# Kernel tuning notes

Measured on AMD Instinct MI355X. Metric: run time of the kernel, lower is better.

Reference implementation:

```python
import jax, jax.numpy as jnp
import numpy as np

N_HIDDEN = 512
BATCH = 16
MAX_LEN = 4096


def setup_inputs() -> dict:
    key = jax.random.key(0)
    k1, k2, k3 = jax.random.split(key, 3)
    h = jax.random.normal(k1, (BATCH, N_HIDDEN, MAX_LEN), dtype=jnp.float32)
    # Conv1d weight [out_ch=3*nh, in_ch=nh, kernel=2], fan-in scaled
    W = jax.random.normal(k2, (3 * N_HIDDEN, N_HIDDEN, 2), dtype=jnp.float32) / np.float32(np.sqrt(2.0 * N_HIDDEN))
    b = 0.02 * jax.random.normal(k3, (3 * N_HIDDEN,), dtype=jnp.float32)
    b = b.at[2 * N_HIDDEN:].set(1.0)  # init_gate_bias on the gate third of the bias
    # lengths: grouped (unique_consecutive) and sorted descending, padded into width MAX_LEN
    N = jnp.array([4096] * 4 + [3000] * 4 + [2048] * 4 + [1000] * 4, dtype=jnp.int32)
    return {"h": h, "W": W, "b": b, "N": N}


def _conv_reduce(h, W, b):
    # _reduce: Conv1d(nh -> 3*nh, kernel=2, stride=2) then gated combine (dropout=0).
    B, C, L = h.shape
    Lp = L + (L % 2)
    x = jnp.pad(h, ((0, 0), (0, 0), (0, Lp - L))).reshape(B, C, Lp // 2, 2)
    lrg = jnp.einsum('bclk,ock->bol', x, W) + b[None, :, None]  # [B, 3C, L//2]
    l = lrg[:, :C]
    r = jnp.tanh(lrg[:, C:2 * C])
    g = jax.nn.sigmoid(lrg[:, 2 * C:])
    return l * g + r * (1.0 - g)


def _forward(h, W, b, N):
    B, nh, L = h.shape
    # Nfp2 = largest power of two <= N ; M = 2*(N - Nfp2)
    Nfp2 = (2 ** jnp.floor(jnp.log2(N.astype(jnp.float32)))).astype(N.dtype)
    M = 2 * (N - Nfp2)
    # --- prefix reduce + suffix cat (padded/masked equivalent of _suffix_cat) ---
    # conv is local (k=2, s=2), so reducing the full padded width gives identical
    # values at the kept positions j < M//2.
    red = _conv_reduce(h, W, b)                      # [B, nh, ceil(L/2)]
    red = jnp.pad(red, ((0, 0), (0, 0), (0, L - red.shape[-1])))
    j = jnp.arange(L)
    half = (M // 2)[:, None]                         # [B, 1]
    take_red = j[None, :] < half                     # first M//2 slots <- reduced prefix
    idx = jnp.where(take_red, j[None, :], jnp.minimum(j[None, :] + half, L - 1))
    suf = jnp.take_along_axis(h, jnp.broadcast_to(idx[:, None, :], (B, nh, L)), axis=2)
    cur = jnp.where(take_red[:, None, :], red, suf)  # per-seq length now Nfp2 (power of 2)
    n = Nfp2
    # --- halving tree reduction; freeze sequences that reached length 1 ---
    steps = int(np.floor(np.log2(L)))
    for _ in range(steps):
        red = _conv_reduce(cur, W, b)
        neww = red.shape[-1]
        active = (n > 1)[:, None, None]
        cur = jnp.where(active, red, cur[:, :, :neww])
        n = jnp.where(n > 1, n // 2, n)
    return cur[:, :, 0]  # squeeze(-1) -> [B, nh]


def reference(h, W, b, N):
    return _forward(h, W, b, N)
```

## Files before the change

### kernel.cpp

```cpp
#include <hip/hip_runtime.h>

#define BATCH 16
#define CH 512
#define OC 1536
#define KDIM 1024
#define LMAX 4096
#define WGLOB_SZ 3145728

typedef __attribute__((ext_vector_type(8))) _Float16 h8v;
typedef __attribute__((ext_vector_type(4))) float f4v;

__device__ __forceinline__ int nfp2_of(int n) { return 1 << (31 - __clz(n)); }

__device__ __forceinline__ unsigned short h2u(_Float16 h) {
  union { _Float16 h; unsigned short u; } v; v.h = h; return v.u;
}

__device__ __forceinline__ void layout(const int* __restrict__ Nvec, int b,
                                       size_t& offC0, size_t& offA, size_t& offB,
                                       int& n, int& nfp2, int& half) {
  size_t c0t = 0, at = 0, bt = 0, c0o = 0, ao = 0, bo = 0;
  n = 2; nfp2 = 2; half = 0;
#pragma unroll 1
  for (int i = 0; i < BATCH; ++i) {
    int ni = Nvec[i];
    int f = nfp2_of(ni);
    int hf = ni - f;
    size_t cs = (size_t)((hf + 127) & ~127) << 11;
    size_t as = (size_t)(f >> 1) << 11;
    size_t bs = (size_t)(f >> 2) << 11;
    if (i < b) { c0o += cs; ao += as; bo += bs; }
    if (i == b) { n = ni; nfp2 = f; half = hf; }
    c0t += cs; at += as; bt += bs;
  }
  offC0 = (size_t)WGLOB_SZ + c0o;
  offA = (size_t)WGLOB_SZ + c0t + ao;
  offB = (size_t)WGLOB_SZ + c0t + at + bo;
}

__device__ __forceinline__ void gload16(const void* g, void* l) {
  __builtin_amdgcn_global_load_lds((const __attribute__((address_space(1))) void*)g,
                                   (__attribute__((address_space(3))) void*)l, 16, 0, 0);
}

__global__ __launch_bounds__(256) void prep_w_k(const float* __restrict__ W, char* __restrict__ ws) {
  int idx = blockIdx.x * 256 + threadIdx.x;
  if (idx >= 16 * 1536) return;
  int step = idx / 1536;
  int o = idx - step * 1536;
  const float* src = W + (size_t)o * KDIM + step * 64;
  unsigned short hb[64];
#pragma unroll
  for (int t = 0; t < 64; ++t) hb[t] = h2u((_Float16)src[t]);
  uint4* d4 = (uint4*)(ws + ((size_t)idx << 7));
#pragma unroll
  for (int s = 0; s < 8; ++s) {
    int oc = (s ^ (o & 7)) * 8;
    uint4 v;
    v.x = (unsigned)hb[oc + 0] | ((unsigned)hb[oc + 1] << 16);
    v.y = (unsigned)hb[oc + 2] | ((unsigned)hb[oc + 3] << 16);
    v.z = (unsigned)hb[oc + 4] | ((unsigned)hb[oc + 5] << 16);
    v.w = (unsigned)hb[oc + 6] | ((unsigned)hb[oc + 7] << 16);
    d4[s] = v;
  }
}

__global__ __launch_bounds__(256) void reorg_h_k(const float* __restrict__ h,
                                                 const int* __restrict__ Nvec,
                                                 char* __restrict__ ws,
                                                 float* __restrict__ dout, int mode) {
  __shared__ char T[32 * 256];
  const int b = blockIdx.z;
  size_t offC0, offA, offB; int n, nfp2, half;
  layout(Nvec, b, offC0, offA, offB, n, nfp2, half);
  const int tid = threadIdx.x;
  const int by = blockIdx.y;
  const int c0 = by * 64;

  if (mode == 1 && nfp2 == 1) {
    if (blockIdx.x == 0 && tid < 64)
      dout[(size_t)b * CH + c0 + tid] = h[(size_t)b * CH * LMAX + (size_t)(c0 + tid) * LMAX];
    return;
  }

  const int d0 = blockIdx.x * 32;
  int dlo, dhi, soff;
  size_t base;
  if (mode == 0) { dlo = 0; dhi = half; soff = 0; base = offC0; }
  else { dlo = half >> 1; dhi = nfp2 >> 1; soff = half; base = offA; }
  if (d0 >= dhi || d0 + 32 <= dlo) return;

  const float* hb = h + (size_t)b * CH * LMAX;

#pragma unroll
  for (int q = 0; q < 8; ++q) {
    int id = q * 256 + tid;
    int cl = id >> 5;
    int dl = id & 31;
    int d = d0 + dl;
    bool ok = (d < dhi) && (d >= dlo);
    float2 v;
    v.x = 0.f; v.y = 0.f;
    if (ok) v = *(const float2*)(hb + (size_t)(c0 + cl) * LMAX + 2 * d + soff);
    unsigned u = (unsigned)h2u((_Float16)v.x) | ((unsigned)h2u((_Float16)v.y) << 16);
    int g = cl >> 2;
    *(unsigned*)(T + dl * 256 + ((g ^ (dl & 15)) << 4) + (cl & 3) * 4) = u;
  }
  __syncthreads();
#pragma unroll
  for (int qq = 0; qq < 2; ++qq) {
    int gid = qq * 256 + tid;
    int dl = gid >> 4;
    int s = gid & 15;
    int d = d0 + dl;
    if (d >= dhi || d < dlo) continue;
    uint4 val = *(const uint4*)(T + dl * 256 + ((s ^ (dl & 15)) << 4));
    size_t dst = base + ((size_t)d << 11) + (size_t)((2 * by + (s >> 3)) << 7) +
                 (((s & 7) ^ (d & 7)) << 4);
    *(uint4*)(ws + dst) = val;
  }
}

__global__ __launch_bounds__(256, 2) void mfma_level_k(const float* __restrict__ bias,
                                                       const int* __restrict__ Nvec,
                                                       char* __restrict__ ws,
                                                       float* __restrict__ dout,
                                                       int level, int tiles) {
  __shared__ char smem[81920];
  const int id = blockIdx.x;
  const int o0 = (id & 7) * 64;
  const int r2 = id >> 3;
  const int xb = r2 % tiles;
  const int b = r2 / tiles;
  if (b >= BATCH) return;

  size_t offC0, offA, offB; int n, nfp2, half;
  layout(Nvec, b, offC0, offA, offB, n, nfp2, half);

  int cols;
  size_t inOff, outOff;
  if (level == 0) {
    if (half == 0) return;
    cols = half;
    inOff = offC0;
    outOff = offA;
  } else {
    int w = nfp2 >> (level - 1);
    if (w < 2) return;
    cols = w >> 1;
    inOff = (level & 1) ? offA : offB;
    outOff = (level & 1) ? offB : offA;
  }
  const bool fin = (level > 0) && ((nfp2 >> level) == 1);
  const int l0 = xb * 128;
  if (l0 >= cols) return;

  const int tid = threadIdx.x;
  const int lane = tid & 63, wid = tid >> 6;
  const int lane15 = lane & 15, lq = lane >> 4;
  const int rg = wid & 1, cg = wid >> 1;
  const char* inp = ws + inOff;

  unsigned aoff[6]; int adst[6];
#pragma unroll
  for (int q = 0; q < 6; ++q) {
    int d = q * 4096 + tid * 16;
    int r = d >> 7;
    int p = d & 127;
    int o = ((r >> 6) << 9) + o0 + (r & 63);
    aoff[q] = ((unsigned)o << 7) + p;
    adst[q] = q * 4096 + wid * 1024;
  }
  unsigned boff[4]; int bdst[4];
#pragma unroll
  for (int q = 0; q < 4; ++q) {
    int d = q * 4096 + tid * 16;
    int l = d >> 7;
    int p = d & 127;
    int lc = l0 + l; if (lc > cols - 1) lc = cols - 1;
    boff[q] = ((unsigned)lc << 11) + p;
    bdst[q] = q * 4096 + wid * 1024;
  }

#define STAGE(st, sel) do {                                                  \
    char* Ab = smem + (sel) * 24576;                                         \
    char* Bb = smem + 49152 + (sel) * 16384;                                 \
    unsigned ka = (unsigned)(st) * 196608u;                                  \
    unsigned kb = (unsigned)(st) << 7;                                       \
    _Pragma("unroll") for (int q = 0; q < 6; ++q)                            \
      gload16(ws + ka + aoff[q], Ab + adst[q]);                              \
    _Pragma("unroll") for (int q = 0; q < 4; ++q)                            \
      gload16(inp + kb + boff[q], Bb + bdst[q]);                             \
  } while (0)

  f4v acc[6][4];
#pragma unroll
  for (int m = 0; m < 6; ++m)
#pragma unroll
    for (int cf = 0; cf < 4; ++cf) acc[m][cf] = (f4v){0.f, 0.f, 0.f, 0.f};

  STAGE(0, 0);
  __syncthreads();

#pragma unroll 1
  for (int st = 0; st < 16; ++st) {
    const int cur = st & 1;
    if (st + 1 < 16) STAGE(st + 1, cur ^ 1);
    const char* Asb = smem + cur * 24576;
    const char* Bsb = smem + 49152 + cur * 16384;

#pragma unroll
    for (int s2 = 0; s2 < 2; ++s2) {
      const int oct = (s2 << 2) | lq;
      h8v bh[4];
#pragma unroll
      for (int cf = 0; cf < 4; ++cf) {
        int ll = cg * 64 + cf * 16 + lane15;
        bh[cf] = *(const h8v*)(Bsb + ll * 128 + ((oct ^ (ll & 7)) << 4));
      }
#pragma unroll
      for (int m = 0; m < 6; ++m) {
        int rr = (m >> 1) * 64 + rg * 32 + (m & 1) * 16 + lane15;
        h8v ah = *(const h8v*)(Asb + rr * 128 + ((oct ^ (rr & 7)) << 4));
#pragma unroll
        for (int cf = 0; cf < 4; ++cf)
          acc[m][cf] = __builtin_amdgcn_mfma_f32_16x16x32_f16(ah, bh[cf], acc[m][cf], 0, 0, 0);
      }
    }
    __syncthreads();
  }
#undef STAGE

  char* outp = ws + outOff;
#pragma unroll
  for (int s = 0; s < 2; ++s) {
#pragma unroll
    for (int cf = 0; cf < 4; ++cf) {
      f4v vl = acc[s][cf], vr = acc[2 + s][cf], vg = acc[4 + s][cf];
      int l = l0 + cg * 64 + cf * 16 + lane15;
      if (l >= cols) continue;
      int P = l >> 1, par = l & 1;
#pragma unroll
      for (int j = 0; j < 4; ++j) {
        int c = o0 + rg * 32 + s * 16 + lq * 4 + j;
        float zl = vl[j] + bias[c];
        float zr = vr[j] + bias[CH + c];
        float zg = vg[j] + bias[2 * CH + c];
        float g = 1.f / (1.f + __expf(-zg));
        float rt = 1.f - 2.f / (1.f + __expf(2.f * zr));
        float val = zl * g + rt * (1.f - g);
        if (fin) {
          if (l == 0) dout[(size_t)b * CH + c] = val;
        } else {
          int k = 2 * c + par;
          size_t byte = ((size_t)P << 11) + (size_t)((k >> 6) << 7) +
                        ((((k >> 3) & 7) ^ (P & 7)) << 4) + ((k & 7) << 1);
          *(unsigned short*)(outp + byte) = h2u((_Float16)val);
        }
      }
    }
  }
}

__global__ __launch_bounds__(256, 2) void small_level_k(const float* __restrict__ bias,
                                                        const int* __restrict__ Nvec,
                                                        char* __restrict__ ws,
                                                        float* __restrict__ dout,
                                                        int level, int tiles) {
  __shared__ char smem[131072];
  const int id = blockIdx.x;
  const int o0 = (id & 7) * 64;
  const int r2 = id >> 3;
  const int xb = r2 % tiles;
  const int b = r2 / tiles;
  if (b >= BATCH) return;

  size_t offC0, offA, offB; int n, nfp2, half;
  layout(Nvec, b, offC0, offA, offB, n, nfp2, half);

  int w = nfp2 >> (level - 1);
  if (w < 2) return;
  const int cols = w >> 1;
  const size_t inOff = (level & 1) ? offA : offB;
  const size_t outOff = (level & 1) ? offB : offA;
  const bool fin = (cols == 1);
  const int l0 = xb * 64;
  if (l0 >= cols) return;

  const int tid = threadIdx.x;
  const int lane = tid & 63, wid = tid >> 6;
  const int lane15 = lane & 15, lq = lane >> 4;
  const int rg = wid & 1, cg = wid >> 1;
  const char* inp = ws + inOff;

  unsigned aoff[12]; int adst[12];
#pragma unroll
  for (int q = 0; q < 12; ++q) {
    int d = q * 4096 + tid * 16;
    int r = d >> 8;
    int p = d & 255;
    int o = ((r >> 6) << 9) + o0 + (r & 63);
    aoff[q] = (unsigned)(p >> 7) * 196608u + ((unsigned)o << 7) + (p & 127);
    adst[q] = q * 4096 + wid * 1024;
  }
  unsigned boff[4]; int bdst[4];
#pragma unroll
  for (int q = 0; q < 4; ++q) {
    int d = q * 4096 + tid * 16;
    int l = d >> 8;
    int p = d & 255;
    int lc = l0 + l; if (lc > cols - 1) lc = cols - 1;
    boff[q] = ((unsigned)lc << 11) + (unsigned)((p >> 7) << 7) + (p & 127);
    bdst[q] = q * 4096 + wid * 1024;
  }

#define STAGES(st, sel) do {                                                 \
    char* Ab = smem + (sel) * 49152;                                         \
    char* Bb = smem + 98304 + (sel) * 16384;                                 \
    unsigned ka = (unsigned)(st) * 393216u;                                  \
    unsigned kb = (unsigned)(st) << 8;                                       \
    _Pragma("unroll") for (int q = 0; q < 12; ++q)                           \
      gload16(ws + ka + aoff[q], Ab + adst[q]);                              \
    _Pragma("unroll") for (int q = 0; q < 4; ++q)                            \
      gload16(inp + kb + boff[q], Bb + bdst[q]);                             \
  } while (0)

  f4v acc[6][2];
#pragma unroll
  for (int m = 0; m < 6; ++m)
#pragma unroll
    for (int cf = 0; cf < 2; ++cf) acc[m][cf] = (f4v){0.f, 0.f, 0.f, 0.f};

  STAGES(0, 0);
  __syncthreads();

#pragma unroll 1
  for (int st = 0; st < 8; ++st) {
    const int cur = st & 1;
    if (st + 1 < 8) STAGES(st + 1, cur ^ 1);
    const char* Asb = smem + cur * 49152;
    const char* Bsb = smem + 98304 + cur * 16384;

#pragma unroll
    for (int sub = 0; sub < 2; ++sub) {
#pragma unroll
      for (int s2 = 0; s2 < 2; ++s2) {
        const int oct = (s2 << 2) | lq;
        h8v bh[2];
#pragma unroll
        for (int cf = 0; cf < 2; ++cf) {
          int ll = cg * 32 + cf * 16 + lane15;
          bh[cf] = *(const h8v*)(Bsb + ll * 256 + sub * 128 + ((oct ^ (ll & 7)) << 4));
        }
#pragma unroll
        for (int m = 0; m < 6; ++m) {
          int rr = (m >> 1) * 64 + rg * 32 + (m & 1) * 16 + lane15;
          h8v ah = *(const h8v*)(Asb + rr * 256 + sub * 128 + ((oct ^ (rr & 7)) << 4));
#pragma unroll
          for (int cf = 0; cf < 2; ++cf)
            acc[m][cf] = __builtin_amdgcn_mfma_f32_16x16x32_f16(ah, bh[cf], acc[m][cf], 0, 0, 0);
        }
      }
    }
    __syncthreads();
  }
#undef STAGES

  char* outp = ws + outOff;
#pragma unroll
  for (int s = 0; s < 2; ++s) {
#pragma unroll
    for (int cf = 0; cf < 2; ++cf) {
      f4v vl = acc[s][cf], vr = acc[2 + s][cf], vg = acc[4 + s][cf];
      int l = l0 + cg * 32 + cf * 16 + lane15;
      if (l >= cols) continue;
      int P = l >> 1, par = l & 1;
#pragma unroll
      for (int j = 0; j < 4; ++j) {
        int c = o0 + rg * 32 + s * 16 + lq * 4 + j;
        float zl = vl[j] + bias[c];
        float zr = vr[j] + bias[CH + c];
        float zg = vg[j] + bias[2 * CH + c];
        float g = 1.f / (1.f + __expf(-zg));
        float rt = 1.f - 2.f / (1.f + __expf(2.f * zr));
        float val = zl * g + rt * (1.f - g);
        if (fin) {
          if (l == 0) dout[(size_t)b * CH + c] = val;
        } else {
          int k = 2 * c + par;
          size_t byte = ((size_t)P << 11) + (size_t)((k >> 6) << 7) +
                        ((((k >> 3) & 7) ^ (P & 7)) << 4) + ((k & 7) << 1);
          *(unsigned short*)(outp + byte) = h2u((_Float16)val);
        }
      }
    }
  }
}

extern "C" void kernel_launch(void* const* d_in, const int* in_sizes, int n_in,
                              void* d_out, int out_size, void* d_ws, size_t ws_size,
                              hipStream_t stream) {
  const float* h = (const float*)d_in[0];
  const float* W = (const float*)d_in[1];
  const float* bias = (const float*)d_in[2];
  const int* Nvec = (const int*)d_in[3];
  float* dout = (float*)d_out;
  char* ws = (char*)d_ws;

  prep_w_k<<<dim3(96), 256, 0, stream>>>(W, ws);
  reorg_h_k<<<dim3(64, 8, BATCH), 256, 0, stream>>>(h, Nvec, ws, dout, 0);
  reorg_h_k<<<dim3(64, 8, BATCH), 256, 0, stream>>>(h, Nvec, ws, dout, 1);

  mfma_level_k<<<dim3(8 * 8 * BATCH), 256, 0, stream>>>(bias, Nvec, ws, dout, 0, 8);
  for (int lev = 1; lev <= 4; ++lev) {
    int tiles = (LMAX >> lev) / 128;
    mfma_level_k<<<dim3(tiles * 8 * BATCH), 256, 0, stream>>>(bias, Nvec, ws, dout, lev, tiles);
  }
  for (int lev = 5; lev <= 12; ++lev) {
    int colsmax = LMAX >> lev;
    int tiles = (colsmax + 63) / 64; if (tiles < 1) tiles = 1;
    small_level_k<<<dim3(tiles * 8 * BATCH), 256, 0, stream>>>(bias, Nvec, ws, dout, lev, tiles);
  }
}
```

Measured before the change: 462.1 us.

## Read weight fragments directly from global memory instead of staging through LDS

Both level GEMM kernels stop copying the weight (A) tile into shared memory and have each lane load its fp16 A fragments straight from global memory, relying on cache. Shared memory per block falls to the B double buffer only, and launch bounds are raised to three blocks per CU to allow more occupancy. This removes the A-tile LDS traffic and the A share of the staging, but puts uncached-latency global loads inside the MFMA inner loop with no prefetch. It also adds register pressure from the per-row pointers.

```diff
diff --git a/kernel.cpp b/kernel.cpp
--- a/kernel.cpp
+++ b/kernel.cpp
@@ -121,12 +121,12 @@
   }
 }
 
-__global__ __launch_bounds__(256, 2) void mfma_level_k(const float* __restrict__ bias,
+__global__ __launch_bounds__(256, 3) void mfma_level_k(const float* __restrict__ bias,
                                                        const int* __restrict__ Nvec,
                                                        char* __restrict__ ws,
                                                        float* __restrict__ dout,
                                                        int level, int tiles) {
-  __shared__ char smem[81920];
+  __shared__ char smem[32768];
   const int id = blockIdx.x;
   const int o0 = (id & 7) * 64;
   const int r2 = id >> 3;
@@ -161,16 +161,6 @@
   const int rg = wid & 1, cg = wid >> 1;
   const char* inp = ws + inOff;
 
-  unsigned aoff[6]; int adst[6];
-#pragma unroll
-  for (int q = 0; q < 6; ++q) {
-    int d = q * 4096 + tid * 16;
-    int r = d >> 7;
-    int p = d & 127;
-    int o = ((r >> 6) << 9) + o0 + (r & 63);
-    aoff[q] = ((unsigned)o << 7) + p;
-    adst[q] = q * 4096 + wid * 1024;
-  }
   unsigned boff[4]; int bdst[4];
 #pragma unroll
   for (int q = 0; q < 4; ++q) {
@@ -182,13 +172,18 @@
     bdst[q] = q * 4096 + wid * 1024;
   }
 
-#define STAGE(st, sel) do {                                                  \
-    char* Ab = smem + (sel) * 24576;                                         \
-    char* Bb = smem + 49152 + (sel) * 16384;                                 \
-    unsigned ka = (unsigned)(st) * 196608u;                                  \
+  const char* ap[6]; int o7[6];
+#pragma unroll
+  for (int m = 0; m < 6; ++m) {
+    int rr = (m >> 1) * 64 + rg * 32 + (m & 1) * 16 + lane15;
+    int o = ((rr >> 6) << 9) + o0 + (rr & 63);
+    ap[m] = ws + ((size_t)o << 7);
+    o7[m] = o & 7;
+  }
+
+#define STAGE_B(st, sel) do {                                                \
+    char* Bb = smem + (sel) * 16384;                                         \
     unsigned kb = (unsigned)(st) << 7;                                       \
-    _Pragma("unroll") for (int q = 0; q < 6; ++q)                            \
-      gload16(ws + ka + aoff[q], Ab + adst[q]);                              \
     _Pragma("unroll") for (int q = 0; q < 4; ++q)                            \
       gload16(inp + kb + boff[q], Bb + bdst[q]);                             \
   } while (0)
@@ -199,15 +194,15 @@
 #pragma unroll
     for (int cf = 0; cf < 4; ++cf) acc[m][cf] = (f4v){0.f, 0.f, 0.f, 0.f};
 
-  STAGE(0, 0);
+  STAGE_B(0, 0);
   __syncthreads();
 
 #pragma unroll 1
   for (int st = 0; st < 16; ++st) {
     const int cur = st & 1;
-    if (st + 1 < 16) STAGE(st + 1, cur ^ 1);
-    const char* Asb = smem + cur * 24576;
-    const char* Bsb = smem + 49152 + cur * 16384;
+    if (st + 1 < 16) STAGE_B(st + 1, cur ^ 1);
+    const char* Bsb = smem + cur * 16384;
+    const unsigned ka = (unsigned)st * 196608u;
 
 #pragma unroll
     for (int s2 = 0; s2 < 2; ++s2) {
@@ -220,8 +215,7 @@
       }
 #pragma unroll
       for (int m = 0; m < 6; ++m) {
-        int rr = (m >> 1) * 64 + rg * 32 + (m & 1) * 16 + lane15;
-        h8v ah = *(const h8v*)(Asb + rr * 128 + ((oct ^ (rr & 7)) << 4));
+        h8v ah = *(const h8v*)(ap[m] + ka + ((oct ^ o7[m]) << 4));
 #pragma unroll
         for (int cf = 0; cf < 4; ++cf)
           acc[m][cf] = __builtin_amdgcn_mfma_f32_16x16x32_f16(ah, bh[cf], acc[m][cf], 0, 0, 0);
@@ -229,7 +223,7 @@
     }
     __syncthreads();
   }
-#undef STAGE
+#undef STAGE_B
 
   char* outp = ws + outOff;
 #pragma unroll
@@ -262,12 +256,12 @@
   }
 }
 
-__global__ __launch_bounds__(256, 2) void small_level_k(const float* __restrict__ bias,
+__global__ __launch_bounds__(256, 3) void small_level_k(const float* __restrict__ bias,
                                                         const int* __restrict__ Nvec,
                                                         char* __restrict__ ws,
                                                         float* __restrict__ dout,
                                                         int level, int tiles) {
-  __shared__ char smem[131072];
+  __shared__ char smem[32768];
   const int id = blockIdx.x;
   const int o0 = (id & 7) * 64;
   const int r2 = id >> 3;
@@ -293,16 +287,6 @@
   const int rg = wid & 1, cg = wid >> 1;
   const char* inp = ws + inOff;
 
-  unsigned aoff[12]; int adst[12];
-#pragma unroll
-  for (int q = 0; q < 12; ++q) {
-    int d = q * 4096 + tid * 16;
-    int r = d >> 8;
-    int p = d & 255;
-    int o = ((r >> 6) << 9) + o0 + (r & 63);
-    aoff[q] = (unsigned)(p >> 7) * 196608u + ((unsigned)o << 7) + (p & 127);
-    adst[q] = q * 4096 + wid * 1024;
-  }
   unsigned boff[4]; int bdst[4];
 #pragma unroll
   for (int q = 0; q < 4; ++q) {
@@ -314,13 +298,18 @@
     bdst[q] = q * 4096 + wid * 1024;
   }
 
-#define STAGES(st, sel) do {                                                 \
-    char* Ab = smem + (sel) * 49152;                                         \
-    char* Bb = smem + 98304 + (sel) * 16384;                                 \
-    unsigned ka = (unsigned)(st) * 393216u;                                  \
+  const char* ap[6]; int o7[6];
+#pragma unroll
+  for (int m = 0; m < 6; ++m) {
+    int rr = (m >> 1) * 64 + rg * 32 + (m & 1) * 16 + lane15;
+    int o = ((rr >> 6) << 9) + o0 + (rr & 63);
+    ap[m] = ws + ((size_t)o << 7);
+    o7[m] = o & 7;
+  }
+
+#define STAGE_BS(st, sel) do {                                               \
+    char* Bb = smem + (sel) * 16384;                                         \
     unsigned kb = (unsigned)(st) << 8;                                       \
-    _Pragma("unroll") for (int q = 0; q < 12; ++q)                           \
-      gload16(ws + ka + aoff[q], Ab + adst[q]);                              \
     _Pragma("unroll") for (int q = 0; q < 4; ++q)                            \
       gload16(inp + kb + boff[q], Bb + bdst[q]);                             \
   } while (0)
@@ -331,18 +320,18 @@
 #pragma unroll
     for (int cf = 0; cf < 2; ++cf) acc[m][cf] = (f4v){0.f, 0.f, 0.f, 0.f};
 
-  STAGES(0, 0);
+  STAGE_BS(0, 0);
   __syncthreads();
 
 #pragma unroll 1
   for (int st = 0; st < 8; ++st) {
     const int cur = st & 1;
-    if (st + 1 < 8) STAGES(st + 1, cur ^ 1);
-    const char* Asb = smem + cur * 49152;
-    const char* Bsb = smem + 98304 + cur * 16384;
+    if (st + 1 < 8) STAGE_BS(st + 1, cur ^ 1);
+    const char* Bsb = smem + cur * 16384;
 
 #pragma unroll
     for (int sub = 0; sub < 2; ++sub) {
+      const unsigned ka = (unsigned)(2 * st + sub) * 196608u;
 #pragma unroll
       for (int s2 = 0; s2 < 2; ++s2) {
         const int oct = (s2 << 2) | lq;
@@ -354,8 +343,7 @@
         }
 #pragma unroll
         for (int m = 0; m < 6; ++m) {
-          int rr = (m >> 1) * 64 + rg * 32 + (m & 1) * 16 + lane15;
-          h8v ah = *(const h8v*)(Asb + rr * 256 + sub * 128 + ((oct ^ (rr & 7)) << 4));
+          h8v ah = *(const h8v*)(ap[m] + ka + ((oct ^ o7[m]) << 4));
 #pragma unroll
           for (int cf = 0; cf < 2; ++cf)
             acc[m][cf] = __builtin_amdgcn_mfma_f32_16x16x32_f16(ah, bh[cf], acc[m][cf], 0, 0, 0);
@@ -364,7 +352,7 @@
     }
     __syncthreads();
   }
-#undef STAGES
+#undef STAGE_BS
 
   char* outp = ws + outOff;
 #pragma unroll
```

Result: slower. 554.0 us (+19.9%).
